# Optimization experiments

Measured on AMD Instinct MI355X. Metric: run time of the kernel, lower is better.

## Reference

```python
import jax, jax.numpy as jnp
import numpy as np

PASSES = 5
NUM_EDGE_SETS = 3
B, N, D = 8, 20000, 128
E = 64000
HID, OUT = 80, 10


def setup_inputs() -> dict:
    key = jax.random.key(0)
    ks = jax.random.split(key, 8)
    nodes = jax.random.normal(ks[0], (B, N, D), dtype=jnp.float32)
    problem_type = jax.random.normal(ks[1], (B, 1), dtype=jnp.float32)
    # edges[b, k, e] = (dst, src); index_add target is column 0, gathered source is column 1
    edges = jax.random.randint(ks[2], (B, NUM_EDGE_SETS, E, 2), 0, N, dtype=jnp.int32)
    w1 = jax.random.normal(ks[3], (D + 1, HID), jnp.float32) / np.sqrt(D + 1).astype(np.float32)
    b1 = jnp.zeros((HID,), jnp.float32)
    w2 = jax.random.normal(ks[4], (HID, HID), jnp.float32) / np.sqrt(HID).astype(np.float32)
    b2 = jnp.zeros((HID,), jnp.float32)
    w3 = jax.random.normal(ks[5], (HID, OUT), jnp.float32) / np.sqrt(HID).astype(np.float32)
    b3 = jnp.zeros((OUT,), jnp.float32)
    return {"nodes": nodes, "problem_type": problem_type, "w1": w1, "b1": b1,
            "w2": w2, "b2": b2, "w3": w3, "b3": b3, "edges": edges}


def _message_pass(nodes_g, edges_g):
    # nodes_g: [N, D]; edges_g: [K, E, 2] with (dst, src)
    inc = jnp.zeros_like(nodes_g)
    for k in range(NUM_EDGE_SETS):  # small fixed set of edge types
        dst = edges_g[k, :, 0]
        src = edges_g[k, :, 1]
        inc = inc + jax.ops.segment_sum(nodes_g[src], dst, num_segments=N)
    return nodes_g + inc


def _forward(nodes, problem_type, w1, b1, w2, b2, w3, b3, edges):
    step = jax.vmap(_message_pass)  # over batch of graphs

    def body(n, _):
        return step(n, edges), None

    nodes, _ = jax.lax.scan(body, nodes, None, length=PASSES)
    pooled = nodes.sum(axis=1)                       # [B, D]
    y = jnp.log(pooled)
    y = jnp.where(jnp.isnan(y), 0.0, y)              # nan -> 0
    y = jax.nn.relu(y)
    finite_max = jnp.max(jnp.where(jnp.isinf(y), -jnp.inf, y), axis=1, keepdims=True)
    y = jnp.where(y == jnp.inf, finite_max, y)       # +inf -> max finite entry
    x = jnp.concatenate([y, problem_type], axis=1)   # [B, D+1]
    x = jax.nn.leaky_relu(x @ w1 + b1)
    x = jax.nn.leaky_relu(x @ w2 + b2)
    return x @ w3 + b3                               # [B, OUT]


def reference(nodes, problem_type, w1, b1, w2, b2, w3, b3, edges):
    return _forward(nodes, problem_type, w1, b1, w2, b2, w3, b3, edges)
```

## Files before the change

### kernel.cpp

```cpp
#include <hip/hip_runtime.h>
#include <cmath>

#define NB 8
#define NN 20000
#define ND 128
#define NE_TOT 192000

#define GSZ 640
#define NG 32
#define FIX 8192
#define KPT 8
#define ECHUNK 8000
#define NCHUNK 24

__device__ float g_w0[NB * NN];
__device__ float g_w1[NB * NN];
__device__ int   g_bcnt[NB][NCHUNK][NG];
__device__ int   g_cnt[NB * NG];
__device__ int2  g_bucket[(size_t)NB * NG * FIX];
__device__ float g_ppart[NB * NG * ND];

__global__ void countK(const int* __restrict__ edges) {
    __shared__ int hist[NG];
    const int b = blockIdx.x / NCHUNK, c = blockIdx.x % NCHUNK;
    const int t = threadIdx.x;
    if (t < NG) hist[t] = 0;
    __syncthreads();
    const int2* __restrict__ ep =
        (const int2*)edges + (size_t)b * NE_TOT + (size_t)c * ECHUNK;
    for (int i = t; i < ECHUNK; i += 256)
        atomicAdd(&hist[(unsigned)ep[i].y / GSZ], 1);
    __syncthreads();
    if (t < NG) g_bcnt[b][c][t] = hist[t];
}

__global__ void distK(const int* __restrict__ edges) {
    __shared__ int cur[NG];
    const int b = blockIdx.x / NCHUNK, c = blockIdx.x % NCHUNK;
    const int t = threadIdx.x;
    if (t < NG) {
        int off = 0;
        for (int cc = 0; cc < c; ++cc) off += g_bcnt[b][cc][t];
        cur[t] = off;
        if (c == NCHUNK - 1) g_cnt[b * NG + t] = off + g_bcnt[b][c][t];
    }
    __syncthreads();
    const int2* __restrict__ ep =
        (const int2*)edges + (size_t)b * NE_TOT + (size_t)c * ECHUNK;
    for (int i = t; i < ECHUNK; i += 256) {
        const int2 e = ep[i];
        const unsigned g = (unsigned)e.y / GSZ;
        const int pos = atomicAdd(&cur[g], 1);
        if (pos < FIX)
            g_bucket[((size_t)(b * NG + g)) * FIX + pos] =
                make_int2(e.x, e.y - (int)g * GSZ);
    }
}

template<bool FIRST>
__global__ void __launch_bounds__(1024)
passK(int sel) {
    extern __shared__ float w_lds[];
    __shared__ float acc[GSZ + 8];
    const int b = blockIdx.y, g = blockIdx.x;
    const int t = threadIdx.x;
    const float* __restrict__ wb = (sel ? g_w1 : g_w0) + b * NN;
    float* __restrict__ wn       = (sel ? g_w0 : g_w1) + b * NN;
    const int cnt = g_cnt[b * NG + g];
    const int2* __restrict__ bk = g_bucket + (size_t)(b * NG + g) * FIX + t;

    int2 e[KPT];
#pragma unroll
    for (int k = 0; k < KPT; ++k) e[k] = bk[k * 1024];

    if (!FIRST) {
        const float4* __restrict__ wb4 = (const float4*)wb;
        for (int i = t; i < NN / 4; i += 1024) ((float4*)w_lds)[i] = wb4[i];
    }
    if (t < GSZ + 8) acc[t] = 0.0f;
    __syncthreads();

#pragma unroll
    for (int k = 0; k < KPT; ++k)
        if (k * 1024 + t < cnt)
            unsafeAtomicAdd(&acc[e[k].y], FIRST ? 1.0f : w_lds[e[k].x]);
    __syncthreads();

    if (t < GSZ) {
        const int node = g * GSZ + t;
        if (node < NN)
            wn[node] = (FIRST ? 1.0f : w_lds[node]) + acc[t];
    }
}

__global__ void __launch_bounds__(1024)
pass5poolK(const float* __restrict__ nodes) {
    extern __shared__ float w_lds[];
    __shared__ float acc[GSZ + 8];
    __shared__ float w5s[GSZ];
    const int b = blockIdx.y, g = blockIdx.x;
    const int t = threadIdx.x;
    const float* __restrict__ wb = g_w0 + b * NN;
    const int cnt = g_cnt[b * NG + g];
    const int2* __restrict__ bk = g_bucket + (size_t)(b * NG + g) * FIX + t;

    int2 e[KPT];
#pragma unroll
    for (int k = 0; k < KPT; ++k) e[k] = bk[k * 1024];

    const float4* __restrict__ wb4 = (const float4*)wb;
    for (int i = t; i < NN / 4; i += 1024) ((float4*)w_lds)[i] = wb4[i];
    if (t < GSZ + 8) acc[t] = 0.0f;
    __syncthreads();

#pragma unroll
    for (int k = 0; k < KPT; ++k)
        if (k * 1024 + t < cnt)
            unsafeAtomicAdd(&acc[e[k].y], w_lds[e[k].x]);
    __syncthreads();

    if (t < GSZ) {
        const int node = g * GSZ + t;
        w5s[t] = (node < NN) ? w_lds[node] + acc[t] : 0.0f;
    }
    __syncthreads();

    const int dslot = t & 31, rg = t >> 5;
    const int nbase = g * GSZ;
    const int nrows = min(GSZ, NN - nbase);
    const float4* __restrict__ base = (const float4*)(nodes + (size_t)b * NN * ND);
    float4 aA = {0.f, 0.f, 0.f, 0.f}, aB = {0.f, 0.f, 0.f, 0.f};
    int row = rg;
    for (; row + 32 < nrows; row += 64) {
        const float wA = w5s[row], wB = w5s[row + 32];
        const float4 vA = base[(size_t)(nbase + row) * 32 + dslot];
        const float4 vB = base[(size_t)(nbase + row + 32) * 32 + dslot];
        aA.x += wA * vA.x; aA.y += wA * vA.y; aA.z += wA * vA.z; aA.w += wA * vA.w;
        aB.x += wB * vB.x; aB.y += wB * vB.y; aB.z += wB * vB.z; aB.w += wB * vB.w;
    }
    if (row < nrows) {
        const float wA = w5s[row];
        const float4 vA = base[(size_t)(nbase + row) * 32 + dslot];
        aA.x += wA * vA.x; aA.y += wA * vA.y; aA.z += wA * vA.z; aA.w += wA * vA.w;
    }
    float4 s4;
    s4.x = aA.x + aB.x; s4.y = aA.y + aB.y; s4.z = aA.z + aB.z; s4.w = aA.w + aB.w;

    __syncthreads();
    float4* red = (float4*)w_lds;
    red[t] = s4;
    __syncthreads();
    if (t < 32) {
        float4 s = red[t];
        for (int q = 1; q < 32; ++q) {
            const float4 o = red[q * 32 + t];
            s.x += o.x; s.y += o.y; s.z += o.z; s.w += o.w;
        }
        ((float4*)g_ppart)[((size_t)b * NG + g) * 32 + t] = s;
    }
}

__global__ void reduceHeadK(const float* __restrict__ ptype,
                            const float* __restrict__ w1, const float* __restrict__ b1,
                            const float* __restrict__ w2, const float* __restrict__ b2,
                            const float* __restrict__ w3, const float* __restrict__ b3,
                            float* __restrict__ out) {
    __shared__ float sx[NB][ND + 1];
    __shared__ float h1s[NB][80];
    __shared__ float h2s[NB][80];
    const int t = threadIdx.x;
    const int b = t >> 7, d = t & 127;

    float s = 0.0f;
    for (int j = 0; j < NG; ++j)
        s += g_ppart[(b * NG + j) * ND + d];

    float y = logf(s);
    if (isnan(y)) y = 0.0f;
    y = fmaxf(y, 0.0f);
    sx[b][d] = y;
    __syncthreads();

    if (t < NB) {
        float fm = -INFINITY;
        for (int dd = 0; dd < ND; ++dd) {
            const float v = sx[t][dd];
            if (!isinf(v)) fm = fmaxf(fm, v);
        }
        for (int dd = 0; dd < ND; ++dd)
            if (isinf(sx[t][dd])) sx[t][dd] = fm;
        sx[t][ND] = ptype[t];
    }
    __syncthreads();

    if (t < NB * 80) {
        const int bb = t / 80, j = t - bb * 80;
        float v = b1[j];
        for (int k = 0; k < ND + 1; ++k) v += sx[bb][k] * w1[k * 80 + j];
        h1s[bb][j] = v > 0.0f ? v : 0.01f * v;
    }
    __syncthreads();

    if (t < NB * 80) {
        const int bb = t / 80, j = t - bb * 80;
        float v = b2[j];
        for (int k = 0; k < 80; ++k) v += h1s[bb][k] * w2[k * 80 + j];
        h2s[bb][j] = v > 0.0f ? v : 0.01f * v;
    }
    __syncthreads();

    if (t < NB * 10) {
        const int bb = t / 10, j = t - bb * 10;
        float v = b3[j];
        for (int k = 0; k < 80; ++k) v += h2s[bb][k] * w3[k * 10 + j];
        out[bb * 10 + j] = v;
    }
}

extern "C" void kernel_launch(void* const* d_in, const int* in_sizes, int n_in,
                              void* d_out, int out_size, void* d_ws, size_t ws_size,
                              hipStream_t stream) {
    const float* nodes = (const float*)d_in[0];
    const float* ptype = (const float*)d_in[1];
    const float* w1    = (const float*)d_in[2];
    const float* b1    = (const float*)d_in[3];
    const float* w2    = (const float*)d_in[4];
    const float* b2    = (const float*)d_in[5];
    const float* w3    = (const float*)d_in[6];
    const float* b3    = (const float*)d_in[7];
    const int*   edges = (const int*)d_in[8];
    float* out = (float*)d_out;

    countK<<<NB * NCHUNK, 256, 0, stream>>>(edges);
    distK<<<NB * NCHUNK, 256, 0, stream>>>(edges);

    passK<true><<<dim3(NG, NB), 1024, 0, stream>>>(0);
    passK<false><<<dim3(NG, NB), 1024, NN * sizeof(float), stream>>>(1);
    passK<false><<<dim3(NG, NB), 1024, NN * sizeof(float), stream>>>(0);
    passK<false><<<dim3(NG, NB), 1024, NN * sizeof(float), stream>>>(1);

    pass5poolK<<<dim3(NG, NB), 1024, NN * sizeof(float), stream>>>(nodes);

    reduceHeadK<<<1, 1024, 0, stream>>>(ptype, w1, b1, w2, b2, w3, b3, out);
}
```

Measured before the change: 130.1 us.

## Build per-node CSR of incoming edges and replace LDS atomic passes with pull gathers

Adds a sort kernel that turns each destination bucket into a CSR layout (row starts plus a source list per node) and computes the first pass's weights directly from in-degree counts. Later passes become one thread per node pulling neighbor weights from global memory, so the full weight vector is no longer copied into LDS and LDS atomics are gone. The pooling kernel uses smaller 256-thread blocks over more node tiles. This trades coalesced LDS-staged reads for scattered global loads and an extra sort kernel with serial scans, and per-thread work now depends on degree.

Measured after the change: 131.6 us. About the same (+1.1%).

```diff
diff --git a/kernel.cpp b/kernel.cpp
--- a/kernel.cpp
+++ b/kernel.cpp
@@ -12,13 +12,19 @@
 #define KPT 8
 #define ECHUNK 8000
 #define NCHUNK 24
+#define MAXRUN 32
+
+#define PBS 256
+#define NPB ((NN + PBS - 1) / PBS)
 
 __device__ float g_w0[NB * NN];
 __device__ float g_w1[NB * NN];
 __device__ int   g_bcnt[NB][NCHUNK][NG];
 __device__ int   g_cnt[NB * NG];
 __device__ int2  g_bucket[(size_t)NB * NG * FIX];
-__device__ float g_ppart[NB * NG * ND];
+__device__ int   g_edst[NB * NE_TOT];
+__device__ int   g_rs[NB][NG * GSZ + 1];
+__device__ float g_ppart[NB * NPB * ND];
 
 __global__ void countK(const int* __restrict__ edges) {
     __shared__ int hist[NG];
@@ -57,106 +63,138 @@
     }
 }
 
-template<bool FIRST>
 __global__ void __launch_bounds__(1024)
-passK(int sel) {
-    extern __shared__ float w_lds[];
-    __shared__ float acc[GSZ + 8];
+sortK() {
+    __shared__ int hist[GSZ];
+    __shared__ int scan[1024];
+    __shared__ int cursor[GSZ];
+    __shared__ int sgbase;
     const int b = blockIdx.y, g = blockIdx.x;
     const int t = threadIdx.x;
-    const float* __restrict__ wb = (sel ? g_w1 : g_w0) + b * NN;
-    float* __restrict__ wn       = (sel ? g_w0 : g_w1) + b * NN;
-    const int cnt = g_cnt[b * NG + g];
+    const int sc = min(g_cnt[b * NG + g], FIX);
+
     const int2* __restrict__ bk = g_bucket + (size_t)(b * NG + g) * FIX + t;
-
     int2 e[KPT];
 #pragma unroll
-    for (int k = 0; k < KPT; ++k) e[k] = bk[k * 1024];
-
-    if (!FIRST) {
-        const float4* __restrict__ wb4 = (const float4*)wb;
-        for (int i = t; i < NN / 4; i += 1024) ((float4*)w_lds)[i] = wb4[i];
-    }
-    if (t < GSZ + 8) acc[t] = 0.0f;
-    __syncthreads();
-
+    for (int k = 0; k < KPT; ++k) {
+        e[k] = bk[k * 1024];
+        if (k * 1024 + t >= sc) e[k].y = -1;
+    }
+
+    for (int i = t; i < GSZ; i += 1024) hist[i] = 0;
+    if (t < NG) scan[t] = min(g_cnt[b * NG + t], FIX);
+    __syncthreads();
+    if (t == 0) {
+        int s = 0;
+        for (int q = 0; q < g; ++q) s += scan[q];
+        sgbase = s;
+    }
 #pragma unroll
     for (int k = 0; k < KPT; ++k)
-        if (k * 1024 + t < cnt)
-            unsafeAtomicAdd(&acc[e[k].y], FIRST ? 1.0f : w_lds[e[k].x]);
-    __syncthreads();
-
+        if (e[k].y >= 0) atomicAdd(&hist[e[k].y], 1);
+    __syncthreads();
+
+    const int v = (t < GSZ) ? hist[t] : 0;
+    scan[t] = v;
+    __syncthreads();
+    for (int off = 1; off < 1024; off <<= 1) {
+        const int u = (t >= off) ? scan[t - off] : 0;
+        __syncthreads();
+        scan[t] += u;
+        __syncthreads();
+    }
+    const int gbase = sgbase;
     if (t < GSZ) {
+        const int start = scan[t] - v;
+        cursor[t] = start;
         const int node = g * GSZ + t;
-        if (node < NN)
-            wn[node] = (FIRST ? 1.0f : w_lds[node]) + acc[t];
-    }
-}
-
-__global__ void __launch_bounds__(1024)
+        g_rs[b][node] = gbase + start;
+        if (node < NN) g_w1[b * NN + node] = 1.0f + (float)v;
+    }
+    __syncthreads();
+
+    int* __restrict__ out = g_edst + b * NE_TOT + gbase;
+#pragma unroll
+    for (int k = 0; k < KPT; ++k)
+        if (e[k].y >= 0) {
+            const int p = atomicAdd(&cursor[e[k].y], 1);
+            out[p] = e[k].x;
+        }
+}
+
+template<int SRC>
+__global__ void __launch_bounds__(256)
+passK() {
+    const int b = blockIdx.y;
+    const int n = blockIdx.x * PBS + threadIdx.x;
+    if (n >= NN) return;
+    const float* __restrict__ wp = (SRC ? g_w1 : g_w0) + b * NN;
+    float* __restrict__ wn       = (SRC ? g_w0 : g_w1) + b * NN;
+    const int s  = g_rs[b][n];
+    const int en = g_rs[b][n + 1];
+    const int* __restrict__ dl = g_edst + b * NE_TOT;
+    float sum = wp[n];
+#pragma unroll
+    for (int j = 0; j < MAXRUN; ++j)
+        if (s + j < en) sum += wp[dl[s + j]];
+    for (int j = MAXRUN; s + j < en; ++j)
+        sum += wp[dl[s + j]];
+    wn[n] = sum;
+}
+
+__global__ void __launch_bounds__(256)
 pass5poolK(const float* __restrict__ nodes) {
-    extern __shared__ float w_lds[];
-    __shared__ float acc[GSZ + 8];
-    __shared__ float w5s[GSZ];
-    const int b = blockIdx.y, g = blockIdx.x;
-    const int t = threadIdx.x;
-    const float* __restrict__ wb = g_w0 + b * NN;
-    const int cnt = g_cnt[b * NG + g];
-    const int2* __restrict__ bk = g_bucket + (size_t)(b * NG + g) * FIX + t;
-
-    int2 e[KPT];
-#pragma unroll
-    for (int k = 0; k < KPT; ++k) e[k] = bk[k * 1024];
-
-    const float4* __restrict__ wb4 = (const float4*)wb;
-    for (int i = t; i < NN / 4; i += 1024) ((float4*)w_lds)[i] = wb4[i];
-    if (t < GSZ + 8) acc[t] = 0.0f;
-    __syncthreads();
-
-#pragma unroll
-    for (int k = 0; k < KPT; ++k)
-        if (k * 1024 + t < cnt)
-            unsafeAtomicAdd(&acc[e[k].y], w_lds[e[k].x]);
-    __syncthreads();
-
-    if (t < GSZ) {
-        const int node = g * GSZ + t;
-        w5s[t] = (node < NN) ? w_lds[node] + acc[t] : 0.0f;
-    }
+    __shared__ float w5s[PBS];
+    __shared__ __align__(16) float4 red[256];
+    const int b = blockIdx.y, p = blockIdx.x;
+    const int t = threadIdx.x;
+    const int n0 = p * PBS;
+    const int n  = n0 + t;
+    const float* __restrict__ wp = g_w0 + b * NN;
+
+    float w5 = 0.0f;
+    if (n < NN) {
+        const int s  = g_rs[b][n];
+        const int en = g_rs[b][n + 1];
+        const int* __restrict__ dl = g_edst + b * NE_TOT;
+        float sum = wp[n];
+#pragma unroll
+        for (int j = 0; j < MAXRUN; ++j)
+            if (s + j < en) sum += wp[dl[s + j]];
+        for (int j = MAXRUN; s + j < en; ++j) sum += wp[dl[s + j]];
+        w5 = sum;
+    }
+    w5s[t] = w5;
     __syncthreads();
 
     const int dslot = t & 31, rg = t >> 5;
-    const int nbase = g * GSZ;
-    const int nrows = min(GSZ, NN - nbase);
+    const int nrows = min(PBS, NN - n0);
     const float4* __restrict__ base = (const float4*)(nodes + (size_t)b * NN * ND);
     float4 aA = {0.f, 0.f, 0.f, 0.f}, aB = {0.f, 0.f, 0.f, 0.f};
     int row = rg;
-    for (; row + 32 < nrows; row += 64) {
-        const float wA = w5s[row], wB = w5s[row + 32];
-        const float4 vA = base[(size_t)(nbase + row) * 32 + dslot];
-        const float4 vB = base[(size_t)(nbase + row + 32) * 32 + dslot];
+    for (; row + 8 < nrows; row += 16) {
+        const float wA = w5s[row], wB = w5s[row + 8];
+        const float4 vA = base[(size_t)(n0 + row) * 32 + dslot];
+        const float4 vB = base[(size_t)(n0 + row + 8) * 32 + dslot];
         aA.x += wA * vA.x; aA.y += wA * vA.y; aA.z += wA * vA.z; aA.w += wA * vA.w;
         aB.x += wB * vB.x; aB.y += wB * vB.y; aB.z += wB * vB.z; aB.w += wB * vB.w;
     }
     if (row < nrows) {
         const float wA = w5s[row];
-        const float4 vA = base[(size_t)(nbase + row) * 32 + dslot];
+        const float4 vA = base[(size_t)(n0 + row) * 32 + dslot];
         aA.x += wA * vA.x; aA.y += wA * vA.y; aA.z += wA * vA.z; aA.w += wA * vA.w;
     }
     float4 s4;
     s4.x = aA.x + aB.x; s4.y = aA.y + aB.y; s4.z = aA.z + aB.z; s4.w = aA.w + aB.w;
-
-    __syncthreads();
-    float4* red = (float4*)w_lds;
     red[t] = s4;
     __syncthreads();
     if (t < 32) {
         float4 s = red[t];
-        for (int q = 1; q < 32; ++q) {
+        for (int q = 1; q < 8; ++q) {
             const float4 o = red[q * 32 + t];
             s.x += o.x; s.y += o.y; s.z += o.z; s.w += o.w;
         }
-        ((float4*)g_ppart)[((size_t)b * NG + g) * 32 + t] = s;
+        ((float4*)g_ppart)[((size_t)b * NPB + p) * 32 + t] = s;
     }
 }
 
@@ -172,8 +210,8 @@
     const int b = t >> 7, d = t & 127;
 
     float s = 0.0f;
-    for (int j = 0; j < NG; ++j)
-        s += g_ppart[(b * NG + j) * ND + d];
+    for (int j = 0; j < NPB; ++j)
+        s += g_ppart[((size_t)b * NPB + j) * ND + d];
 
     float y = logf(s);
     if (isnan(y)) y = 0.0f;
@@ -233,13 +271,12 @@
 
     countK<<<NB * NCHUNK, 256, 0, stream>>>(edges);
     distK<<<NB * NCHUNK, 256, 0, stream>>>(edges);
-
-    passK<true><<<dim3(NG, NB), 1024, 0, stream>>>(0);
-    passK<false><<<dim3(NG, NB), 1024, NN * sizeof(float), stream>>>(1);
-    passK<false><<<dim3(NG, NB), 1024, NN * sizeof(float), stream>>>(0);
-    passK<false><<<dim3(NG, NB), 1024, NN * sizeof(float), stream>>>(1);
-
-    pass5poolK<<<dim3(NG, NB), 1024, NN * sizeof(float), stream>>>(nodes);
-
+    sortK<<<dim3(NG, NB), 1024, 0, stream>>>();
+
+    passK<1><<<dim3(NPB, NB), PBS, 0, stream>>>();
+    passK<0><<<dim3(NPB, NB), PBS, 0, stream>>>();
+    passK<1><<<dim3(NPB, NB), PBS, 0, stream>>>();
+
+    pass5poolK<<<dim3(NPB, NB), PBS, 0, stream>>>(nodes);
     reduceHeadK<<<1, 1024, 0, stream>>>(ptype, w1, b1, w2, b2, w3, b3, out);
 }
```
